# Performance work log

Measured on AMD Instinct MI355X. Metric: run time of the kernel, lower is better.

## Reference

```python
import jax, jax.numpy as jnp
import numpy as np

N_NODES = 50000

def _gcn_layer(h, src, dst, norm, W, activate):
    # symmetric-normalized aggregation: D^-1/2 A D^-1/2 h, then linear
    h = h * norm[:, None]                      # [N, d] pre-scale
    msg = h[src]                               # gather over edges [E, d]
    agg = jax.ops.segment_sum(msg, dst, num_segments=N_NODES)  # scatter-add
    h = agg * norm[:, None]                    # post-scale
    h = h @ W
    return jax.nn.relu(h) if activate else h


def setup_inputs() -> dict:
    key = jax.random.key(0)
    k1, k2, k3, k4, k5, k6 = jax.random.split(key, 6)
    d_in, d_hid, d_out, n_edges = 128, 128, 40, 640000
    features = jax.random.normal(k1, (N_NODES, d_in), dtype=jnp.float32)
    edge_index = jax.random.randint(k2, (2, n_edges), 0, N_NODES, dtype=jnp.int64)
    s = 1.0 / np.sqrt(d_hid)
    W0 = jax.random.normal(k3, (d_in, d_hid), dtype=jnp.float32) * s
    W1 = jax.random.normal(k4, (d_hid, d_hid), dtype=jnp.float32) * s
    W2 = jax.random.normal(k5, (d_hid, d_hid), dtype=jnp.float32) * s
    W3 = jax.random.normal(k6, (d_hid, d_out), dtype=jnp.float32) * s
    return {"features": features, "edge_index": edge_index,
            "W0": W0, "W1": W1, "W2": W2, "W3": W3}


def reference(features, edge_index, W0, W1, W2, W3):
    src, dst = edge_index[0], edge_index[1]
    # in-degree based symmetric norm (graph_norm=True), clamp isolated nodes
    deg = jax.ops.segment_sum(jnp.ones_like(dst, dtype=features.dtype), dst,
                              num_segments=N_NODES)
    norm = jax.lax.rsqrt(jnp.maximum(deg, 1.0))
    h = features
    h = _gcn_layer(h, src, dst, norm, W0, True)
    h = _gcn_layer(h, src, dst, norm, W1, True)
    h = _gcn_layer(h, src, dst, norm, W2, True)
    h = _gcn_layer(h, src, dst, norm, W3, False)  # last layer: no activation
    return h
```

## Files before the change

kernel.cpp:

```cpp
#include <hip/hip_runtime.h>
#include <hip/hip_fp16.h>


#define DIM 128
#define CHUNK 1024

__global__ void deg_kernel(const int* __restrict__ dst, int* __restrict__ deg, int E) {
    int i = blockIdx.x * blockDim.x + threadIdx.x;
    if (i < E) atomicAdd(&deg[dst[i]], 1);
}

__global__ __launch_bounds__(256) void scanA_kernel(
        const int* __restrict__ deg, float* __restrict__ nrm,
        int* __restrict__ bsum, int n) {
    int b = blockIdx.x, t = threadIdx.x;
    int base = b * CHUNK + t * 4;
    int s = 0;
    if (base + 3 < n) {
        int4 d = *(const int4*)&deg[base];
        s = d.x + d.y + d.z + d.w;
        float4 r;
        r.x = rsqrtf(fmaxf((float)d.x, 1.0f));
        r.y = rsqrtf(fmaxf((float)d.y, 1.0f));
        r.z = rsqrtf(fmaxf((float)d.z, 1.0f));
        r.w = rsqrtf(fmaxf((float)d.w, 1.0f));
        *(float4*)&nrm[base] = r;
    } else {
        for (int j = 0; j < 4; ++j) {
            int idx = base + j;
            if (idx < n) {
                int d = deg[idx];
                s += d;
                nrm[idx] = rsqrtf(fmaxf((float)d, 1.0f));
            }
        }
    }
    for (int o = 32; o; o >>= 1) s += __shfl_down(s, o, 64);
    __shared__ int ws[4];
    if ((t & 63) == 0) ws[t >> 6] = s;
    __syncthreads();
    if (t == 0) bsum[b] = ws[0] + ws[1] + ws[2] + ws[3];
}

__global__ __launch_bounds__(256) void scanBC_kernel(
        const int* __restrict__ deg, const int* __restrict__ bsum,
        int* __restrict__ off, int* __restrict__ cur, int n, int G) {
    __shared__ int pbs;
    __shared__ int wsum[4];
    int b = blockIdx.x, t = threadIdx.x;
    if (t < 64) {
        int orig = (t < G) ? bsum[t] : 0;
        int v = orig;
        for (int o = 1; o < 64; o <<= 1) {
            int u = __shfl_up(v, o, 64);
            if (t >= o) v += u;
        }
        if (b == 0 && t == G - 1) off[n] = v;
        if (t == b) pbs = v - orig;
    }
    int base = b * CHUNK + t * 4;
    if (base + 3 < n) *(int4*)&cur[base] = make_int4(0, 0, 0, 0);
    else for (int j = 0; j < 4; ++j) if (base + j < n) cur[base + j] = 0;

    int d0 = 0, d1 = 0, d2 = 0, d3 = 0;
    if (base + 3 < n) {
        int4 d = *(const int4*)&deg[base];
        d0 = d.x; d1 = d.y; d2 = d.z; d3 = d.w;
    } else {
        if (base     < n) d0 = deg[base];
        if (base + 1 < n) d1 = deg[base + 1];
        if (base + 2 < n) d2 = deg[base + 2];
    }
    int tot = d0 + d1 + d2 + d3;
    int v = tot;
    for (int o = 1; o < 64; o <<= 1) {
        int u = __shfl_up(v, o, 64);
        if ((t & 63) >= o) v += u;
    }
    if ((t & 63) == 63) wsum[t >> 6] = v;
    __syncthreads();
    int wbase = 0;
    for (int w = 0; w < (t >> 6); ++w) wbase += wsum[w];
    int p = pbs + wbase + (v - tot);
    if (base + 3 < n) {
        int4 o4 = make_int4(p, p + d0, p + d0 + d1, p + d0 + d1 + d2);
        *(int4*)&off[base] = o4;
    } else {
        if (base     < n) off[base]     = p;
        if (base + 1 < n) off[base + 1] = p + d0;
        if (base + 2 < n) off[base + 2] = p + d0 + d1;
    }
}

__global__ void fill_kernel(const int* __restrict__ src, const int* __restrict__ dst,
                            const int* __restrict__ off, int* __restrict__ cur,
                            int* __restrict__ csr, int E) {
    int i = blockIdx.x * blockDim.x + threadIdx.x;
    if (i < E) {
        int d = dst[i];
        int p = atomicAdd(&cur[d], 1);
        csr[off[d] + p] = src[i];
    }
}

__global__ void conv_kernel(const float* __restrict__ f, const float* __restrict__ nrm,
                            __half* __restrict__ out, int n4) {
    int i = blockIdx.x * blockDim.x + threadIdx.x;
    if (i < n4) {
        int r = i >> 5, c4 = i & 31;
        float s = nrm[r];
        float4 v = ((const float4*)f)[i];
        __half2 lo = __float22half2_rn(make_float2(v.x * s, v.y * s));
        __half2 hi = __float22half2_rn(make_float2(v.z * s, v.w * s));
        uint2 u;
        u.x = *(unsigned int*)&lo;
        u.y = *(unsigned int*)&hi;
        *(uint2*)&out[(size_t)r * DIM + c4 * 4] = u;
    }
}

__global__ __launch_bounds__(256) void aggh_kernel(
        const __half* __restrict__ hin, const float* __restrict__ nrm,
        const int* __restrict__ off, const int* __restrict__ csr,
        __half* __restrict__ out, int N) {
    int t = threadIdx.x;
    int lane = t & 63;
    int node = blockIdx.x * 4 + (t >> 6);
    if (node >= N) return;
    int pos = lane & 15, sg = lane >> 4;
    int c = pos * 8;
    int b = off[node], e = off[node + 1];
    float a[8] = {0,0,0,0,0,0,0,0};
    float bb[8] = {0,0,0,0,0,0,0,0};
    int j = b + sg;
    for (; j + 4 < e; j += 8) {
        int s0 = csr[j], s1 = csr[j + 4];
        uint4 u0 = *(const uint4*)&hin[(size_t)s0 * DIM + c];
        uint4 u1 = *(const uint4*)&hin[(size_t)s1 * DIM + c];
        float2 f;
        f = __half22float2(*(__half2*)&u0.x); a[0]+=f.x; a[1]+=f.y;
        f = __half22float2(*(__half2*)&u0.y); a[2]+=f.x; a[3]+=f.y;
        f = __half22float2(*(__half2*)&u0.z); a[4]+=f.x; a[5]+=f.y;
        f = __half22float2(*(__half2*)&u0.w); a[6]+=f.x; a[7]+=f.y;
        f = __half22float2(*(__half2*)&u1.x); bb[0]+=f.x; bb[1]+=f.y;
        f = __half22float2(*(__half2*)&u1.y); bb[2]+=f.x; bb[3]+=f.y;
        f = __half22float2(*(__half2*)&u1.z); bb[4]+=f.x; bb[5]+=f.y;
        f = __half22float2(*(__half2*)&u1.w); bb[6]+=f.x; bb[7]+=f.y;
    }
    for (; j < e; j += 4) {
        uint4 u = *(const uint4*)&hin[(size_t)csr[j] * DIM + c];
        float2 f;
        f = __half22float2(*(__half2*)&u.x); a[0]+=f.x; a[1]+=f.y;
        f = __half22float2(*(__half2*)&u.y); a[2]+=f.x; a[3]+=f.y;
        f = __half22float2(*(__half2*)&u.z); a[4]+=f.x; a[5]+=f.y;
        f = __half22float2(*(__half2*)&u.w); a[6]+=f.x; a[7]+=f.y;
    }
#pragma unroll
    for (int k = 0; k < 8; ++k) a[k] += bb[k];
#pragma unroll
    for (int k = 0; k < 8; ++k) {
        a[k] += __shfl_xor(a[k], 16, 64);
        a[k] += __shfl_xor(a[k], 32, 64);
    }
    if (sg == 0) {
        float s = nrm[node];
        __half2 h0 = __float22half2_rn(make_float2(a[0]*s, a[1]*s));
        __half2 h1 = __float22half2_rn(make_float2(a[2]*s, a[3]*s));
        __half2 h2 = __float22half2_rn(make_float2(a[4]*s, a[5]*s));
        __half2 h3 = __float22half2_rn(make_float2(a[6]*s, a[7]*s));
        uint4 u;
        u.x = *(unsigned int*)&h0; u.y = *(unsigned int*)&h1;
        u.z = *(unsigned int*)&h2; u.w = *(unsigned int*)&h3;
        *(uint4*)&out[(size_t)node * DIM + c] = u;
    }
}

__global__ __launch_bounds__(256) void gemm_kernel(
        const __half* __restrict__ Ah, const float* __restrict__ W,
        const float* __restrict__ nrm, __half* __restrict__ outh, int n) {
    __shared__ float As[64 * DIM];
    int t = threadIdx.x;
    int row0 = blockIdx.x * 64;

    for (int q = t; q < 64 * 32; q += 256) {
        int r = q >> 5, c4 = q & 31;
        int row = row0 + r;
        float4 v = make_float4(0.f, 0.f, 0.f, 0.f);
        if (row < n) {
            uint2 u = *(const uint2*)&Ah[(size_t)row * DIM + c4 * 4];
            float2 f0 = __half22float2(*(__half2*)&u.x);
            float2 f1 = __half22float2(*(__half2*)&u.y);
            v = make_float4(f0.x, f0.y, f1.x, f1.y);
        }
        *(float4*)&As[r * DIM + c4 * 4] = v;
    }
    __syncthreads();

    int tc = t & 31, tr = t >> 5;
    float acc[8][4];
#pragma unroll
    for (int i = 0; i < 8; ++i)
#pragma unroll
        for (int j = 0; j < 4; ++j) acc[i][j] = 0.f;

    for (int k4 = 0; k4 < 32; ++k4) {
        float w[4][4];
#pragma unroll
        for (int dk = 0; dk < 4; ++dk) {
            float4 wv4 = *(const float4*)&W[(size_t)(k4 * 4 + dk) * DIM + tc * 4];
            w[dk][0] = wv4.x; w[dk][1] = wv4.y; w[dk][2] = wv4.z; w[dk][3] = wv4.w;
        }
#pragma unroll
        for (int i = 0; i < 8; ++i) {
            float4 a = *(const float4*)&As[(tr * 8 + i) * DIM + k4 * 4];
            float av[4] = {a.x, a.y, a.z, a.w};
#pragma unroll
            for (int dk = 0; dk < 4; ++dk)
#pragma unroll
                for (int j = 0; j < 4; ++j)
                    acc[i][j] += av[dk] * w[dk][j];
        }
    }

#pragma unroll
    for (int i = 0; i < 8; ++i) {
        int row = row0 + tr * 8 + i;
        if (row >= n) continue;
        float s = nrm[row];
        float4 v = make_float4(acc[i][0], acc[i][1], acc[i][2], acc[i][3]);
        v.x = fmaxf(v.x, 0.f) * s; v.y = fmaxf(v.y, 0.f) * s;
        v.z = fmaxf(v.z, 0.f) * s; v.w = fmaxf(v.w, 0.f) * s;
        __half2 lo = __float22half2_rn(make_float2(v.x, v.y));
        __half2 hi = __float22half2_rn(make_float2(v.z, v.w));
        uint2 u;
        u.x = *(unsigned int*)&lo;
        u.y = *(unsigned int*)&hi;
        *(uint2*)&outh[(size_t)row * DIM + tc * 4] = u;
    }
}

__global__ __launch_bounds__(256) void gemm3_kernel(
        const __half* __restrict__ Ah, const float* __restrict__ W,
        __half* __restrict__ outh, int n, int outw) {
    __shared__ float As[64 * DIM];
    int t = threadIdx.x;
    int row0 = blockIdx.x * 64;
    for (int q = t; q < 64 * 32; q += 256) {
        int r = q >> 5, c4 = q & 31;
        int row = row0 + r;
        float4 v = make_float4(0.f, 0.f, 0.f, 0.f);
        if (row < n) {
            uint2 u = *(const uint2*)&Ah[(size_t)row * DIM + c4 * 4];
            float2 f0 = __half22float2(*(__half2*)&u.x);
            float2 f1 = __half22float2(*(__half2*)&u.y);
            v = make_float4(f0.x, f0.y, f1.x, f1.y);
        }
        *(float4*)&As[r * DIM + c4 * 4] = v;
    }
    __syncthreads();

    int tc = t & 31, tr = t >> 5;
    if (tc >= 10) return;
    float acc[8][4];
#pragma unroll
    for (int i = 0; i < 8; ++i)
#pragma unroll
        for (int j = 0; j < 4; ++j) acc[i][j] = 0.f;

    for (int k4 = 0; k4 < 32; ++k4) {
        float w[4][4];
#pragma unroll
        for (int dk = 0; dk < 4; ++dk) {
            float4 wv4 = *(const float4*)&W[(size_t)(k4 * 4 + dk) * outw + tc * 4];
            w[dk][0] = wv4.x; w[dk][1] = wv4.y; w[dk][2] = wv4.z; w[dk][3] = wv4.w;
        }
#pragma unroll
        for (int i = 0; i < 8; ++i) {
            float4 a = *(const float4*)&As[(tr * 8 + i) * DIM + k4 * 4];
            float av[4] = {a.x, a.y, a.z, a.w};
#pragma unroll
            for (int dk = 0; dk < 4; ++dk)
#pragma unroll
                for (int j = 0; j < 4; ++j)
                    acc[i][j] += av[dk] * w[dk][j];
        }
    }

#pragma unroll
    for (int i = 0; i < 8; ++i) {
        int row = row0 + tr * 8 + i;
        if (row >= n) continue;
        __half2 lo = __float22half2_rn(make_float2(acc[i][0], acc[i][1]));
        __half2 hi = __float22half2_rn(make_float2(acc[i][2], acc[i][3]));
        uint2 u;
        u.x = *(unsigned int*)&lo;
        u.y = *(unsigned int*)&hi;
        *(uint2*)&outh[(size_t)row * outw + tc * 4] = u;
    }
}

__global__ __launch_bounds__(256) void agg40_kernel(
        const __half* __restrict__ hin, const float* __restrict__ nrm,
        const int* __restrict__ off, const int* __restrict__ csr,
        float* __restrict__ out, int N) {
    int t = threadIdx.x;
    int lane = t & 63, wv = t >> 6;
    int g = lane >> 4, pos = lane & 15;
    int node = blockIdx.x * 16 + wv * 4 + g;
    if (node >= N || pos >= 10) return;
    int b = off[node], e = off[node + 1];
    float4 a0 = make_float4(0,0,0,0), a1 = a0, a2 = a0, a3 = a0;
    int j = b;
    for (; j + 3 < e; j += 4) {
        int s0 = csr[j], s1 = csr[j+1], s2 = csr[j+2], s3 = csr[j+3];
        uint2 u0 = *(const uint2*)&hin[(size_t)s0 * 40 + pos * 4];
        uint2 u1 = *(const uint2*)&hin[(size_t)s1 * 40 + pos * 4];
        uint2 u2 = *(const uint2*)&hin[(size_t)s2 * 40 + pos * 4];
        uint2 u3 = *(const uint2*)&hin[(size_t)s3 * 40 + pos * 4];
        float2 f;
        f = __half22float2(*(__half2*)&u0.x); a0.x+=f.x; a0.y+=f.y;
        f = __half22float2(*(__half2*)&u0.y); a0.z+=f.x; a0.w+=f.y;
        f = __half22float2(*(__half2*)&u1.x); a1.x+=f.x; a1.y+=f.y;
        f = __half22float2(*(__half2*)&u1.y); a1.z+=f.x; a1.w+=f.y;
        f = __half22float2(*(__half2*)&u2.x); a2.x+=f.x; a2.y+=f.y;
        f = __half22float2(*(__half2*)&u2.y); a2.z+=f.x; a2.w+=f.y;
        f = __half22float2(*(__half2*)&u3.x); a3.x+=f.x; a3.y+=f.y;
        f = __half22float2(*(__half2*)&u3.y); a3.z+=f.x; a3.w+=f.y;
    }
    for (; j < e; ++j) {
        uint2 u = *(const uint2*)&hin[(size_t)csr[j] * 40 + pos * 4];
        float2 f;
        f = __half22float2(*(__half2*)&u.x); a0.x+=f.x; a0.y+=f.y;
        f = __half22float2(*(__half2*)&u.y); a0.z+=f.x; a0.w+=f.y;
    }
    float s = nrm[node];
    float4 r;
    r.x = ((a0.x+a1.x) + (a2.x+a3.x)) * s;
    r.y = ((a0.y+a1.y) + (a2.y+a3.y)) * s;
    r.z = ((a0.z+a1.z) + (a2.z+a3.z)) * s;
    r.w = ((a0.w+a1.w) + (a2.w+a3.w)) * s;
    *(float4*)&out[(size_t)node * 40 + pos * 4] = r;
}

extern "C" void kernel_launch(void* const* d_in, const int* in_sizes, int n_in,
                              void* d_out, int out_size, void* d_ws, size_t ws_size,
                              hipStream_t stream) {
    const float* features = (const float*)d_in[0];
    const int*   edges    = (const int*)d_in[1];
    const float* W0       = (const float*)d_in[2];
    const float* W1       = (const float*)d_in[3];
    const float* W2       = (const float*)d_in[4];
    const float* W3       = (const float*)d_in[5];

    const int N = in_sizes[0] / DIM;
    const int E = in_sizes[1] / 2;
    const int DOUT = out_size / N;
    const int* src = edges;
    const int* dst = edges + E;

    char* p = (char*)d_ws;
    __half* featH = (__half*)p; p += (size_t)N * DIM * 2;
    __half* agg16 = (__half*)p; p += (size_t)N * DIM * 2;
    __half* h16   = (__half*)p; p += (size_t)N * DIM * 2;
    __half* g3h   = (__half*)p; p += (size_t)N * 64 * 2;
    float*  nrm   = (float*)p;  p += (size_t)N * 4;
    int*    deg   = (int*)p;    p += (size_t)N * 4;
    int*    cur   = (int*)p;    p += (size_t)N * 4;
    int*    off   = (int*)p;    p += (size_t)(N + 1) * 4;
    int*    bsum  = (int*)p;    p += 64 * 4;
    int*    csr   = (int*)p;    p += (size_t)E * 4;
    (void)ws_size; (void)n_in;

    hipMemsetAsync(deg, 0, (size_t)N * sizeof(int), stream);

    int eb = (E + 255) / 256;
    int G  = (N + CHUNK - 1) / CHUNK;
    deg_kernel   <<<eb, 256, 0, stream>>>(dst, deg, E);
    scanA_kernel <<<G, 256, 0, stream>>>(deg, nrm, bsum, N);
    scanBC_kernel<<<G, 256, 0, stream>>>(deg, bsum, off, cur, N, G);
    fill_kernel  <<<eb, 256, 0, stream>>>(src, dst, off, cur, csr, E);

    int n4 = N * (DIM / 4);
    conv_kernel<<<(n4 + 255) / 256, 256, 0, stream>>>(features, nrm, featH, n4);

    int gb = (N + 63) / 64;
    int ab = (N + 3) / 4;
    aggh_kernel<<<ab, 256, 0, stream>>>(featH, nrm, off, csr, agg16, N);
    gemm_kernel<<<gb, 256, 0, stream>>>(agg16, W0, nrm, h16, N);

    aggh_kernel<<<ab, 256, 0, stream>>>(h16, nrm, off, csr, agg16, N);
    gemm_kernel<<<gb, 256, 0, stream>>>(agg16, W1, nrm, h16, N);

    aggh_kernel<<<ab, 256, 0, stream>>>(h16, nrm, off, csr, agg16, N);
    gemm_kernel<<<gb, 256, 0, stream>>>(agg16, W2, nrm, h16, N);

    gemm3_kernel<<<gb, 256, 0, stream>>>(h16, W3, g3h, N, DOUT);
    agg40_kernel<<<(N + 15) / 16, 256, 0, stream>>>(g3h, nrm, off, csr,
                                                    (float*)d_out, N);
}
```

Before: 298.3 us.

## Replace FP32 SIMT GEMMs with fp16 MFMA matrix-core kernels

Swaps the shared-memory FP32 FMA GEMMs for kernels that use MFMA 16x16x32 fp16 instructions. A and B fragments are loaded straight from global memory into registers. A new kernel converts the weights to transposed fp16 once per call, with W3 padded to 48 columns. The aim is to cut the compute time of the four dense layers, at the cost of fp16 weight precision and narrower scattered 2-byte output stores.

```diff
diff --git a/kernel.cpp b/kernel.cpp
--- a/kernel.cpp
+++ b/kernel.cpp
@@ -4,6 +4,9 @@
 
 #define DIM 128
 #define CHUNK 1024
+
+typedef __attribute__((ext_vector_type(8))) _Float16 f16x8;
+typedef __attribute__((ext_vector_type(4))) float f32x4;
 
 __global__ void deg_kernel(const int* __restrict__ dst, int* __restrict__ deg, int E) {
     int i = blockIdx.x * blockDim.x + threadIdx.x;
@@ -116,6 +119,22 @@
         u.x = *(unsigned int*)&lo;
         u.y = *(unsigned int*)&hi;
         *(uint2*)&out[(size_t)r * DIM + c4 * 4] = u;
+    }
+}
+
+__global__ void convW_kernel(const float* __restrict__ W0, const float* __restrict__ W1,
+                             const float* __restrict__ W2, const float* __restrict__ W3,
+                             __half* __restrict__ Wt) {
+    int i = blockIdx.x * blockDim.x + threadIdx.x;
+    if (i < 3 * 128 * 128) {
+        int l = i >> 14;
+        int c = (i >> 7) & 127, k = i & 127;
+        const float* W = (l == 0) ? W0 : ((l == 1) ? W1 : W2);
+        Wt[i] = __float2half(W[k * 128 + c]);
+    } else if (i < 3 * 128 * 128 + 48 * 128) {
+        int j = i - 3 * 128 * 128;
+        int c = j >> 7, k = j & 127;
+        Wt[i] = __float2half((c < 40) ? W3[k * 40 + c] : 0.f);
     }
 }
 
@@ -175,127 +194,89 @@
     }
 }
 
-__global__ __launch_bounds__(256) void gemm_kernel(
-        const __half* __restrict__ Ah, const float* __restrict__ W,
+__global__ __launch_bounds__(256) void gemmM_kernel(
+        const __half* __restrict__ Ah, const __half* __restrict__ Wt,
         const float* __restrict__ nrm, __half* __restrict__ outh, int n) {
-    __shared__ float As[64 * DIM];
     int t = threadIdx.x;
-    int row0 = blockIdx.x * 64;
-
-    for (int q = t; q < 64 * 32; q += 256) {
-        int r = q >> 5, c4 = q & 31;
-        int row = row0 + r;
-        float4 v = make_float4(0.f, 0.f, 0.f, 0.f);
-        if (row < n) {
-            uint2 u = *(const uint2*)&Ah[(size_t)row * DIM + c4 * 4];
-            float2 f0 = __half22float2(*(__half2*)&u.x);
-            float2 f1 = __half22float2(*(__half2*)&u.y);
-            v = make_float4(f0.x, f0.y, f1.x, f1.y);
-        }
-        *(float4*)&As[r * DIM + c4 * 4] = v;
-    }
-    __syncthreads();
-
-    int tc = t & 31, tr = t >> 5;
-    float acc[8][4];
-#pragma unroll
-    for (int i = 0; i < 8; ++i)
-#pragma unroll
-        for (int j = 0; j < 4; ++j) acc[i][j] = 0.f;
-
-    for (int k4 = 0; k4 < 32; ++k4) {
-        float w[4][4];
-#pragma unroll
-        for (int dk = 0; dk < 4; ++dk) {
-            float4 wv4 = *(const float4*)&W[(size_t)(k4 * 4 + dk) * DIM + tc * 4];
-            w[dk][0] = wv4.x; w[dk][1] = wv4.y; w[dk][2] = wv4.z; w[dk][3] = wv4.w;
-        }
-#pragma unroll
-        for (int i = 0; i < 8; ++i) {
-            float4 a = *(const float4*)&As[(tr * 8 + i) * DIM + k4 * 4];
-            float av[4] = {a.x, a.y, a.z, a.w};
-#pragma unroll
-            for (int dk = 0; dk < 4; ++dk)
-#pragma unroll
-                for (int j = 0; j < 4; ++j)
-                    acc[i][j] += av[dk] * w[dk][j];
-        }
-    }
-
-#pragma unroll
-    for (int i = 0; i < 8; ++i) {
-        int row = row0 + tr * 8 + i;
+    int lane = t & 63, wv = t >> 6;
+    int row0 = blockIdx.x * 64 + wv * 16;
+    int arow = row0 + (lane & 15);
+    int ar = (arow < n) ? arow : (n - 1);
+    int kg = lane >> 4;
+
+    const __half* Abase = Ah + (size_t)ar * DIM + kg * 8;
+    f16x8 a[4];
+#pragma unroll
+    for (int k0 = 0; k0 < 4; ++k0)
+        a[k0] = *(const f16x8*)(Abase + k0 * 32);
+
+    f32x4 acc[8];
+#pragma unroll
+    for (int ct = 0; ct < 8; ++ct) {
+        acc[ct] = (f32x4){0.f, 0.f, 0.f, 0.f};
+        const __half* Bbase = Wt + (size_t)(ct * 16 + (lane & 15)) * DIM + kg * 8;
+#pragma unroll
+        for (int k0 = 0; k0 < 4; ++k0) {
+            f16x8 b = *(const f16x8*)(Bbase + k0 * 32);
+            acc[ct] = __builtin_amdgcn_mfma_f32_16x16x32_f16(a[k0], b, acc[ct], 0, 0, 0);
+        }
+    }
+
+    int col = lane & 15;
+    int rbase = row0 + (lane >> 4) * 4;
+#pragma unroll
+    for (int r = 0; r < 4; ++r) {
+        int row = rbase + r;
         if (row >= n) continue;
         float s = nrm[row];
-        float4 v = make_float4(acc[i][0], acc[i][1], acc[i][2], acc[i][3]);
-        v.x = fmaxf(v.x, 0.f) * s; v.y = fmaxf(v.y, 0.f) * s;
-        v.z = fmaxf(v.z, 0.f) * s; v.w = fmaxf(v.w, 0.f) * s;
-        __half2 lo = __float22half2_rn(make_float2(v.x, v.y));
-        __half2 hi = __float22half2_rn(make_float2(v.z, v.w));
-        uint2 u;
-        u.x = *(unsigned int*)&lo;
-        u.y = *(unsigned int*)&hi;
-        *(uint2*)&outh[(size_t)row * DIM + tc * 4] = u;
-    }
-}
-
-__global__ __launch_bounds__(256) void gemm3_kernel(
-        const __half* __restrict__ Ah, const float* __restrict__ W,
-        __half* __restrict__ outh, int n, int outw) {
-    __shared__ float As[64 * DIM];
+#pragma unroll
+        for (int ct = 0; ct < 8; ++ct) {
+            float v = fmaxf(acc[ct][r], 0.f) * s;
+            outh[(size_t)row * DIM + ct * 16 + col] = __float2half(v);
+        }
+    }
+}
+
+__global__ __launch_bounds__(256) void gemm3M_kernel(
+        const __half* __restrict__ Ah, const __half* __restrict__ Wt3,
+        __half* __restrict__ outh, int n) {
     int t = threadIdx.x;
-    int row0 = blockIdx.x * 64;
-    for (int q = t; q < 64 * 32; q += 256) {
-        int r = q >> 5, c4 = q & 31;
-        int row = row0 + r;
-        float4 v = make_float4(0.f, 0.f, 0.f, 0.f);
-        if (row < n) {
-            uint2 u = *(const uint2*)&Ah[(size_t)row * DIM + c4 * 4];
-            float2 f0 = __half22float2(*(__half2*)&u.x);
-            float2 f1 = __half22float2(*(__half2*)&u.y);
-            v = make_float4(f0.x, f0.y, f1.x, f1.y);
-        }
-        *(float4*)&As[r * DIM + c4 * 4] = v;
-    }
-    __syncthreads();
-
-    int tc = t & 31, tr = t >> 5;
-    if (tc >= 10) return;
-    float acc[8][4];
-#pragma unroll
-    for (int i = 0; i < 8; ++i)
-#pragma unroll
-        for (int j = 0; j < 4; ++j) acc[i][j] = 0.f;
-
-    for (int k4 = 0; k4 < 32; ++k4) {
-        float w[4][4];
-#pragma unroll
-        for (int dk = 0; dk < 4; ++dk) {
-            float4 wv4 = *(const float4*)&W[(size_t)(k4 * 4 + dk) * outw + tc * 4];
-            w[dk][0] = wv4.x; w[dk][1] = wv4.y; w[dk][2] = wv4.z; w[dk][3] = wv4.w;
-        }
-#pragma unroll
-        for (int i = 0; i < 8; ++i) {
-            float4 a = *(const float4*)&As[(tr * 8 + i) * DIM + k4 * 4];
-            float av[4] = {a.x, a.y, a.z, a.w};
-#pragma unroll
-            for (int dk = 0; dk < 4; ++dk)
-#pragma unroll
-                for (int j = 0; j < 4; ++j)
-                    acc[i][j] += av[dk] * w[dk][j];
-        }
-    }
-
-#pragma unroll
-    for (int i = 0; i < 8; ++i) {
-        int row = row0 + tr * 8 + i;
+    int lane = t & 63, wv = t >> 6;
+    int row0 = blockIdx.x * 64 + wv * 16;
+    int arow = row0 + (lane & 15);
+    int ar = (arow < n) ? arow : (n - 1);
+    int kg = lane >> 4;
+
+    const __half* Abase = Ah + (size_t)ar * DIM + kg * 8;
+    f16x8 a[4];
+#pragma unroll
+    for (int k0 = 0; k0 < 4; ++k0)
+        a[k0] = *(const f16x8*)(Abase + k0 * 32);
+
+    f32x4 acc[3];
+#pragma unroll
+    for (int ct = 0; ct < 3; ++ct) {
+        acc[ct] = (f32x4){0.f, 0.f, 0.f, 0.f};
+        const __half* Bbase = Wt3 + (size_t)(ct * 16 + (lane & 15)) * DIM + kg * 8;
+#pragma unroll
+        for (int k0 = 0; k0 < 4; ++k0) {
+            f16x8 b = *(const f16x8*)(Bbase + k0 * 32);
+            acc[ct] = __builtin_amdgcn_mfma_f32_16x16x32_f16(a[k0], b, acc[ct], 0, 0, 0);
+        }
+    }
+
+    int col = lane & 15;
+    int rbase = row0 + (lane >> 4) * 4;
+#pragma unroll
+    for (int r = 0; r < 4; ++r) {
+        int row = rbase + r;
         if (row >= n) continue;
-        __half2 lo = __float22half2_rn(make_float2(acc[i][0], acc[i][1]));
-        __half2 hi = __float22half2_rn(make_float2(acc[i][2], acc[i][3]));
-        uint2 u;
-        u.x = *(unsigned int*)&lo;
-        u.y = *(unsigned int*)&hi;
-        *(uint2*)&outh[(size_t)row * outw + tc * 4] = u;
+#pragma unroll
+        for (int ct = 0; ct < 3; ++ct) {
+            int cc = ct * 16 + col;
+            if (cc < 40)
+                outh[(size_t)row * 40 + cc] = __float2half(acc[ct][r]);
+        }
     }
 }
 
@@ -354,7 +335,6 @@
 
     const int N = in_sizes[0] / DIM;
     const int E = in_sizes[1] / 2;
-    const int DOUT = out_size / N;
     const int* src = edges;
     const int* dst = edges + E;
 
@@ -363,6 +343,7 @@
     __half* agg16 = (__half*)p; p += (size_t)N * DIM * 2;
     __half* h16   = (__half*)p; p += (size_t)N * DIM * 2;
     __half* g3h   = (__half*)p; p += (size_t)N * 64 * 2;
+    __half* Wt    = (__half*)p; p += (size_t)(3 * 128 * 128 + 48 * 128) * 2;
     float*  nrm   = (float*)p;  p += (size_t)N * 4;
     int*    deg   = (int*)p;    p += (size_t)N * 4;
     int*    cur   = (int*)p;    p += (size_t)N * 4;
@@ -380,21 +361,24 @@
     scanBC_kernel<<<G, 256, 0, stream>>>(deg, bsum, off, cur, N, G);
     fill_kernel  <<<eb, 256, 0, stream>>>(src, dst, off, cur, csr, E);
 
+    int wB = (3 * 128 * 128 + 48 * 128 + 255) / 256;
+    convW_kernel<<<wB, 256, 0, stream>>>(W0, W1, W2, W3, Wt);
+
     int n4 = N * (DIM / 4);
     conv_kernel<<<(n4 + 255) / 256, 256, 0, stream>>>(features, nrm, featH, n4);
 
     int gb = (N + 63) / 64;
     int ab = (N + 3) / 4;
     aggh_kernel<<<ab, 256, 0, stream>>>(featH, nrm, off, csr, agg16, N);
-    gemm_kernel<<<gb, 256, 0, stream>>>(agg16, W0, nrm, h16, N);
+    gemmM_kernel<<<gb, 256, 0, stream>>>(agg16, Wt, nrm, h16, N);
 
     aggh_kernel<<<ab, 256, 0, stream>>>(h16, nrm, off, csr, agg16, N);
-    gemm_kernel<<<gb, 256, 0, stream>>>(agg16, W1, nrm, h16, N);
+    gemmM_kernel<<<gb, 256, 0, stream>>>(agg16, Wt + 128 * 128, nrm, h16, N);
 
     aggh_kernel<<<ab, 256, 0, stream>>>(h16, nrm, off, csr, agg16, N);
-    gemm_kernel<<<gb, 256, 0, stream>>>(agg16, W2, nrm, h16, N);
-
-    gemm3_kernel<<<gb, 256, 0, stream>>>(h16, W3, g3h, N, DOUT);
+    gemmM_kernel<<<gb, 256, 0, stream>>>(agg16, Wt + 2 * 128 * 128, nrm, h16, N);
+
+    gemm3M_kernel<<<gb, 256, 0, stream>>>(h16, Wt + 3 * 128 * 128, g3h, N);
     agg40_kernel<<<(N + 15) / 16, 256, 0, stream>>>(g3h, nrm, off, csr,
                                                     (float*)d_out, N);
 }
```

Result: faster. 261.4 us (-12.4%).
